# Kernel tuning notes

Measured on AMD Instinct MI355X. Metric: run time of the kernel, lower is better.

## Reference

```python
import jax, jax.numpy as jnp
import numpy as np
import math

MAX2D = 1001        # max_2d_position_embeddings
COORD = 128         # coordinate_size
SHAPE = 128         # shape_size
PE = 384            # pos_embed_size
HID = 768           # layout_hidden_size
PAD = 0             # pad_token_id
EPS = 1e-12
INIT = 1024         # sinusoidal init_size
BIG = 100000000


def sinusoidal_table(num_embeddings=INIT, dim=PE, padding_idx=PAD):
    half = dim // 2
    freq = np.exp(np.arange(half, dtype=np.float32) * (-math.log(10000.0) / (half - 1)))
    ang = np.arange(num_embeddings, dtype=np.float32)[:, None] * freq[None, :]
    tab = np.concatenate([np.sin(ang), np.cos(ang)], axis=1)
    if padding_idx is not None:
        tab[padding_idx, :] = 0.0
    return jnp.asarray(tab, dtype=jnp.float32)


def setup_inputs() -> dict:
    key = jax.random.key(0)
    ks = jax.random.split(key, 16)
    B, L = 2, 1024
    x1 = jax.random.randint(ks[0], (B, L), 0, 501, dtype=jnp.int32)
    y1 = jax.random.randint(ks[1], (B, L), 0, 501, dtype=jnp.int32)
    w = jax.random.randint(ks[2], (B, L), 0, 500, dtype=jnp.int32)
    h = jax.random.randint(ks[3], (B, L), 0, 500, dtype=jnp.int32)
    bbox = jnp.stack([x1, y1, x1 + w, y1 + h], axis=-1)  # [B,L,4], 0..1000
    attention_mask = jnp.ones((B, L), dtype=jnp.int32)
    s = 0.02
    inp = {
        'bbox': bbox,
        'attention_mask': attention_mask,
        'x_tab': jax.random.normal(ks[4], (MAX2D, COORD), jnp.float32) * s,
        'y_tab': jax.random.normal(ks[5], (MAX2D, COORD), jnp.float32) * s,
        'h_tab': jax.random.normal(ks[6], (MAX2D, SHAPE), jnp.float32) * s,
        'w_tab': jax.random.normal(ks[7], (MAX2D, SHAPE), jnp.float32) * s,
        'W_tl_w': jax.random.normal(ks[8], (HID, 2 * PE), jnp.float32) * s,
        'W_tl_b': jnp.zeros((HID,), jnp.float32),
        'W_tr_w': jax.random.normal(ks[9], (HID, 2 * PE), jnp.float32) * s,
        'W_tr_b': jnp.zeros((HID,), jnp.float32),
        'W_bl_w': jax.random.normal(ks[10], (HID, 2 * PE), jnp.float32) * s,
        'W_bl_b': jnp.zeros((HID,), jnp.float32),
        'W_br_w': jax.random.normal(ks[11], (HID, 2 * PE), jnp.float32) * s,
        'W_br_b': jnp.zeros((HID,), jnp.float32),
        'ln_g': jnp.ones((HID,), jnp.float32),
        'ln_b': jnp.zeros((HID,), jnp.float32),
        'params': 50,
    }
    return inp


def _knn_graph(bbox, mask, topk):
    # mask out padded boxes with a huge coordinate (matches masked_fill)
    bm = jnp.where((mask == 0)[..., None], BIG, bbox).astype(jnp.float32)
    xc = (bm[:, :, 0] + bm[:, :, 2]) / 2.0
    yc = (bm[:, :, 1] + bm[:, :, 3]) / 2.0
    dist = (xc[:, :, None] - xc[:, None, :]) ** 2 + (yc[:, :, None] - yc[:, None, :]) ** 2
    _, topk_index = jax.lax.top_k(-dist, topk)  # smallest distances
    topk_index = topk_index.astype(jnp.int32)
    B, L, _ = topk_index.shape
    lm = jnp.zeros((B, L, L), jnp.int32)
    b_ix = jnp.arange(B)[:, None, None]
    l_ix = jnp.arange(L)[None, :, None]
    lm = lm.at[b_ix, l_ix, topk_index].set(1)
    return topk_index, lm


def _rel_pos_emb(bbox, topk_index, sin_tab):
    # diff[b,i,k] = coord[b,i] - coord[b,topk_index[b,i,k]]
    gather = jax.vmap(lambda v, idx: v[idx])  # per-batch gather

    def diffs(c):
        d = c[:, :, None] - gather(c, topk_index)
        d = jnp.clip(d, 1 - MAX2D, MAX2D - 1)
        # torch negative indexing into the table wraps: idx % INIT
        return sin_tab[jnp.mod(d, INIT)]  # [B,L,K,PE]

    ex1 = diffs(bbox[:, :, 0])
    ey1 = diffs(bbox[:, :, 1])
    ex2 = diffs(bbox[:, :, 2])
    ey2 = diffs(bbox[:, :, 3])
    return ex1, ey1, ex2, ey2


def _linear(x, w, b):
    return jnp.einsum('blki,oi->blko', x, w) + b


def reference(bbox, attention_mask, x_tab, y_tab, h_tab, w_tab,
              W_tl_w, W_tl_b, W_tr_w, W_tr_b, W_bl_w, W_bl_b, W_br_w, W_br_b,
              ln_g, ln_b, params):
    sin_tab = sinusoidal_table()
    # spatial position embeddings
    layout_emb = jnp.concatenate([
        x_tab[bbox[:, :, 0]], y_tab[bbox[:, :, 1]],
        x_tab[bbox[:, :, 2]], y_tab[bbox[:, :, 3]],
        h_tab[bbox[:, :, 3] - bbox[:, :, 1]],
        w_tab[bbox[:, :, 2] - bbox[:, :, 0]],
    ], axis=-1)  # [B,L,HID]

    topk = min(bbox.shape[1], int(params))
    topk_index, local_mask = _knn_graph(bbox, attention_mask, topk)

    ex1, ey1, ex2, ey2 = _rel_pos_emb(bbox, topk_index, sin_tab)
    p = (_linear(jnp.concatenate([ex1, ey1], -1), W_tl_w, W_tl_b)
         + _linear(jnp.concatenate([ex2, ey1], -1), W_tr_w, W_tr_b)
         + _linear(jnp.concatenate([ex1, ey2], -1), W_bl_w, W_bl_b)
         + _linear(jnp.concatenate([ex2, ey2], -1), W_br_w, W_br_b))

    mu = jnp.mean(layout_emb, axis=-1, keepdims=True)
    var = jnp.mean((layout_emb - mu) ** 2, axis=-1, keepdims=True)
    layout_emb = (layout_emb - mu) / jnp.sqrt(var + EPS) * ln_g + ln_b
    # dropout is identity in eval mode
    return layout_emb, p, topk_index, local_mask
```

## Files before the change

kernel.cpp:

```cpp
#include <hip/hip_runtime.h>
#include <math.h>

namespace {
constexpr int B_ = 2;
constexpr int L_ = 1024;
constexpr int K_ = 50;
constexpr int HID_ = 768;
constexpr int PE_ = 384;
constexpr int HALF_ = 192;
constexpr int TROWS_ = 1024;

typedef float f32x4 __attribute__((ext_vector_type(4)));

constexpr long long OUT0 = 0;
constexpr long long OUT1 = OUT0 + (long long)B_ * L_ * HID_;
constexpr long long OUT2 = OUT1 + (long long)B_ * L_ * K_ * HID_;
constexpr long long OUT3 = OUT2 + (long long)B_ * L_ * K_;

constexpr long long WS_SIN = 0;
constexpr long long WS_T   = WS_SIN + (long long)TROWS_ * PE_;
constexpr long long WS_TI  = WS_T + 4LL * TROWS_ * HID_;

constexpr int GEMM_BLOCKS = 16 * 12 * 4;
constexpr int TOPK_BLOCKS = B_ * L_;
constexpr int LN_BLOCKS   = B_ * L_;
}

__global__ __launch_bounds__(192) void k_sin_tab(float* __restrict__ tab) {
    const int r = blockIdx.x;
    const int j = threadIdx.x;
    const float c = -0.04822168780092243f;
    float fr = expf((float)j * c);
    float ang = (float)r * fr;
    float s, co;
    if (r == 0) { s = 0.f; co = 0.f; } else { s = sinf(ang); co = cosf(ang); }
    tab[r * PE_ + j] = s;
    tab[r * PE_ + HALF_ + j] = co;
}

union SMem {
    struct { float As[32][68]; float Bs[32][68]; } g;
    struct { float xs[L_]; float ys[L_]; float mrow[L_];
             unsigned long long wmin[4]; } t;
    struct { float red[4]; } l;
};

__device__ __forceinline__ float block_sum_256(float x, float* red) {
    #pragma unroll
    for (int off = 32; off > 0; off >>= 1) x += __shfl_xor(x, off, 64);
    const int wave = threadIdx.x >> 6;
    if ((threadIdx.x & 63) == 0) red[wave] = x;
    __syncthreads();
    float t = red[0] + red[1] + red[2] + red[3];
    __syncthreads();
    return t;
}

__global__ __launch_bounds__(256) void k_mega(
    const float* __restrict__ sinT,
    const float* __restrict__ Wtl, const float* __restrict__ Wtr,
    const float* __restrict__ Wbl, const float* __restrict__ Wbr,
    const float* __restrict__ btl, const float* __restrict__ btr,
    const float* __restrict__ bbl, const float* __restrict__ bbr,
    float* __restrict__ Tout,
    const int4* __restrict__ bbox, const int* __restrict__ am,
    float* __restrict__ topk_f, int* __restrict__ topk_i, float* __restrict__ mask,
    const float* __restrict__ xt, const float* __restrict__ yt,
    const float* __restrict__ ht, const float* __restrict__ wt,
    const float* __restrict__ lng, const float* __restrict__ lnb,
    float* __restrict__ lout)
{
    __shared__ SMem sm;
    const int bid = blockIdx.x;
    const int tid = threadIdx.x;

    if (bid < GEMM_BLOCKS) {
        const int t   = bid / 192;
        const int rem = bid - t * 192;
        const int rx  = rem & 15;
        const int oy  = rem >> 4;
        const float* Wa; const float* Wb; int coff;
        if (t == 0)      { Wa = Wtl; Wb = Wbl; coff = 0; }
        else if (t == 1) { Wa = Wtr; Wb = Wbr; coff = 0; }
        else if (t == 2) { Wa = Wtl; Wb = Wtr; coff = PE_; }
        else             { Wa = Wbl; Wb = Wbr; coff = PE_; }

        const int r0 = rx * 64;
        const int o0 = oy * 64;
        const int ty = tid >> 4, tx = tid & 15;
        float acc[4][4] = {{0.f,0.f,0.f,0.f},{0.f,0.f,0.f,0.f},
                           {0.f,0.f,0.f,0.f},{0.f,0.f,0.f,0.f}};

        for (int k0 = 0; k0 < PE_; k0 += 32) {
            #pragma unroll
            for (int s = 0; s < 2; ++s) {
                int idx = s * 256 + tid;
                int rr = idx >> 3, q = idx & 7;
                f32x4 av = *(const f32x4*)&sinT[(r0 + rr) * PE_ + k0 + q * 4];
                f32x4 w1 = *(const f32x4*)&Wa[(o0 + rr) * (2 * PE_) + coff + k0 + q * 4];
                f32x4 w2 = *(const f32x4*)&Wb[(o0 + rr) * (2 * PE_) + coff + k0 + q * 4];
                f32x4 bv = w1 + w2;
                #pragma unroll
                for (int c = 0; c < 4; ++c) {
                    sm.g.As[q * 4 + c][rr] = av[c];
                    sm.g.Bs[q * 4 + c][rr] = bv[c];
                }
            }
            __syncthreads();
            #pragma unroll
            for (int kk = 0; kk < 32; ++kk) {
                f32x4 a = *(const f32x4*)&sm.g.As[kk][ty * 4];
                f32x4 b = *(const f32x4*)&sm.g.Bs[kk][tx * 4];
                #pragma unroll
                for (int m = 0; m < 4; ++m)
                    #pragma unroll
                    for (int n = 0; n < 4; ++n)
                        acc[m][n] = fmaf(a[m], b[n], acc[m][n]);
            }
            __syncthreads();
        }

        #pragma unroll
        for (int m = 0; m < 4; ++m) {
            int r = r0 + ty * 4 + m;
            f32x4 v;
            #pragma unroll
            for (int n = 0; n < 4; ++n) {
                int o = o0 + tx * 4 + n;
                float x = acc[m][n];
                if (t == 0) x += btl[o] + btr[o] + bbl[o] + bbr[o];
                v[n] = x;
            }
            *(f32x4*)&Tout[(long long)t * TROWS_ * HID_ + (long long)r * HID_ + o0 + tx * 4] = v;
        }
        return;
    }

    if (bid < GEMM_BLOCKS + TOPK_BLOCKS) {
        const int bi = bid - GEMM_BLOCKS;
        const int b = bi >> 10;
        const int i = bi & 1023;
        for (int j = tid; j < L_; j += 256) {
            int4 q = bbox[b * L_ + j];
            float x1, y1, x2, y2;
            if (am[b * L_ + j] == 0) { x1 = y1 = x2 = y2 = 1e8f; }
            else { x1 = (float)q.x; y1 = (float)q.y; x2 = (float)q.z; y2 = (float)q.w; }
            sm.t.xs[j] = (x1 + x2) * 0.5f;
            sm.t.ys[j] = (y1 + y2) * 0.5f;
            sm.t.mrow[j] = 0.f;
        }
        __syncthreads();
        const float xq = sm.t.xs[i], yq = sm.t.ys[i];
        unsigned long long key[4];
        #pragma unroll
        for (int s = 0; s < 4; ++s) {
            int j = tid + s * 256;
            float dx = xq - sm.t.xs[j], dy = yq - sm.t.ys[j];
            float d = dx * dx + dy * dy;
            key[s] = ((unsigned long long)__float_as_uint(d) << 32) | (unsigned int)j;
        }
        const int lane = tid & 63, wave = tid >> 6;
        const long long obase = (long long)(b * L_ + i) * K_;
        for (int r = 0; r < K_; ++r) {
            unsigned long long m = key[0] < key[1] ? key[0] : key[1];
            unsigned long long m2 = key[2] < key[3] ? key[2] : key[3];
            if (m2 < m) m = m2;
            #pragma unroll
            for (int off = 1; off < 64; off <<= 1) {
                unsigned long long o = __shfl_xor(m, off, 64);
                if (o < m) m = o;
            }
            if (lane == 0) sm.t.wmin[wave] = m;
            __syncthreads();
            unsigned long long mm = sm.t.wmin[0] < sm.t.wmin[1] ? sm.t.wmin[0] : sm.t.wmin[1];
            unsigned long long mb = sm.t.wmin[2] < sm.t.wmin[3] ? sm.t.wmin[2] : sm.t.wmin[3];
            if (mb < mm) mm = mb;
            if (tid == 0) {
                int w = (int)(mm & 0xffffffffu);
                topk_f[obase + r] = (float)w;
                topk_i[obase + r] = w;
                sm.t.mrow[w] = 1.0f;
            }
            #pragma unroll
            for (int s = 0; s < 4; ++s) if (key[s] == mm) key[s] = ~0ULL;
            __syncthreads();
        }
        f32x4* mrow = (f32x4*)(mask + (long long)(b * L_ + i) * L_);
        const f32x4* src = (const f32x4*)sm.t.mrow;
        __builtin_nontemporal_store(src[tid], mrow + tid);
        return;
    }

    {
        const int tok = bid - (GEMM_BLOCKS + TOPK_BLOCKS);
        const int4 q = bbox[tok];
        float v[3];
        #pragma unroll
        for (int s = 0; s < 3; ++s) {
            int e = tid + s * 256;
            int off = e & 127;
            int seg = e >> 7;
            float val;
            if (seg == 0)      val = xt[q.x * 128 + off];
            else if (seg == 1) val = yt[q.y * 128 + off];
            else if (seg == 2) val = xt[q.z * 128 + off];
            else if (seg == 3) val = yt[q.w * 128 + off];
            else if (seg == 4) val = ht[(q.w - q.y) * 128 + off];
            else               val = wt[(q.z - q.x) * 128 + off];
            v[s] = val;
        }
        float mu = block_sum_256(v[0] + v[1] + v[2], sm.l.red) * (1.0f / 768.0f);
        float sq = 0.f;
        #pragma unroll
        for (int s = 0; s < 3; ++s) { float d = v[s] - mu; sq = fmaf(d, d, sq); }
        float var = block_sum_256(sq, sm.l.red) * (1.0f / 768.0f);
        float inv = 1.0f / sqrtf(var + 1e-12f);
        float* orow = lout + (long long)tok * HID_;
        #pragma unroll
        for (int s = 0; s < 3; ++s) {
            int e = tid + s * 256;
            __builtin_nontemporal_store((v[s] - mu) * inv * lng[e] + lnb[e], orow + e);
        }
    }
}

__device__ __forceinline__ int wrapc(int d) {
    d = d < -1000 ? -1000 : (d > 1000 ? 1000 : d);
    return (d + 1024) & 1023;
}

__global__ __launch_bounds__(256) void k_passemble(
    const int4* __restrict__ bbox, const int* __restrict__ topk_i,
    const f32x4* __restrict__ T, float* __restrict__ p)
{
    const int row = blockIdx.x * 4 + (threadIdx.x >> 6);
    const int lane = threadIdx.x & 63;
    const int b = row / (L_ * K_);
    const int rem = row - b * (L_ * K_);
    const int i = rem / K_;
    const int j = topk_i[row];
    const int4 bi = bbox[b * L_ + i];
    const int4 bj = bbox[b * L_ + j];
    const f32x4* T1 = T + (long long)wrapc(bi.x - bj.x) * 192;
    const f32x4* T2 = T + 196608 + (long long)wrapc(bi.z - bj.z) * 192;
    const f32x4* T3 = T + 2 * 196608 + (long long)wrapc(bi.y - bj.y) * 192;
    const f32x4* T4 = T + 3 * 196608 + (long long)wrapc(bi.w - bj.w) * 192;
    f32x4* prow = (f32x4*)p + (long long)row * 192;
    #pragma unroll
    for (int u = 0; u < 3; ++u) {
        int f = lane + u * 64;
        f32x4 o = T1[f] + T2[f] + T3[f] + T4[f];
        __builtin_nontemporal_store(o, prow + f);
    }
}

extern "C" void kernel_launch(void* const* d_in, const int* in_sizes, int n_in,
                              void* d_out, int out_size, void* d_ws, size_t ws_size,
                              hipStream_t stream)
{
    const int4* bbox = (const int4*)d_in[0];
    const int* am    = (const int*)d_in[1];
    const float* xt  = (const float*)d_in[2];
    const float* yt  = (const float*)d_in[3];
    const float* ht  = (const float*)d_in[4];
    const float* wt  = (const float*)d_in[5];
    const float* Wtl = (const float*)d_in[6];
    const float* btl = (const float*)d_in[7];
    const float* Wtr = (const float*)d_in[8];
    const float* btr = (const float*)d_in[9];
    const float* Wbl = (const float*)d_in[10];
    const float* bbl = (const float*)d_in[11];
    const float* Wbr = (const float*)d_in[12];
    const float* bbr = (const float*)d_in[13];
    const float* lng = (const float*)d_in[14];
    const float* lnb = (const float*)d_in[15];

    float* out = (float*)d_out;
    float* ws = (float*)d_ws;
    float* sinT = ws + WS_SIN;
    float* T = ws + WS_T;
    int* topk_i = (int*)(ws + WS_TI);

    k_sin_tab<<<dim3(TROWS_), dim3(HALF_), 0, stream>>>(sinT);
    k_mega<<<dim3(GEMM_BLOCKS + TOPK_BLOCKS + LN_BLOCKS), dim3(256), 0, stream>>>(
        sinT, Wtl, Wtr, Wbl, Wbr, btl, btr, bbl, bbr, T,
        bbox, am, out + OUT2, topk_i, out + OUT3,
        xt, yt, ht, wt, lng, lnb, out + OUT0);
    k_passemble<<<dim3(B_ * L_ * K_ / 4), dim3(256), 0, stream>>>(
        bbox, topk_i, (const f32x4*)T, out + OUT1);
}
```

Before: 528.4 us.

## Store relative-position tables in fp16 and restructure GEMM with pre-transposed operands

```diff
diff --git a/kernel.cpp b/kernel.cpp
--- a/kernel.cpp
+++ b/kernel.cpp
@@ -11,35 +11,80 @@
 constexpr int TROWS_ = 1024;
 
 typedef float f32x4 __attribute__((ext_vector_type(4)));
+typedef _Float16 f16x4 __attribute__((ext_vector_type(4)));
+typedef _Float16 f16x8 __attribute__((ext_vector_type(8)));
 
 constexpr long long OUT0 = 0;
 constexpr long long OUT1 = OUT0 + (long long)B_ * L_ * HID_;
 constexpr long long OUT2 = OUT1 + (long long)B_ * L_ * K_ * HID_;
 constexpr long long OUT3 = OUT2 + (long long)B_ * L_ * K_;
 
-constexpr long long WS_SIN = 0;
-constexpr long long WS_T   = WS_SIN + (long long)TROWS_ * PE_;
-constexpr long long WS_TI  = WS_T + 4LL * TROWS_ * HID_;
-
-constexpr int GEMM_BLOCKS = 16 * 12 * 4;
+constexpr long long WS_ST = 0;
+constexpr long long WS_UT = WS_ST + (long long)PE_ * TROWS_;
+constexpr long long WS_T  = WS_UT + 4LL * PE_ * HID_;
+constexpr long long WS_TI = WS_T + 2LL * TROWS_ * HID_;
+
+constexpr int GEMM_BLOCKS = 8 * 6 * 4;
 constexpr int TOPK_BLOCKS = B_ * L_;
 constexpr int LN_BLOCKS   = B_ * L_;
 }
 
-__global__ __launch_bounds__(192) void k_sin_tab(float* __restrict__ tab) {
-    const int r = blockIdx.x;
-    const int j = threadIdx.x;
-    const float c = -0.04822168780092243f;
-    float fr = expf((float)j * c);
-    float ang = (float)r * fr;
-    float s, co;
-    if (r == 0) { s = 0.f; co = 0.f; } else { s = sinf(ang); co = cosf(ang); }
-    tab[r * PE_ + j] = s;
-    tab[r * PE_ + HALF_ + j] = co;
-}
-
-union SMem {
-    struct { float As[32][68]; float Bs[32][68]; } g;
+__global__ __launch_bounds__(256) void k_pre(
+    const float* __restrict__ Wtl, const float* __restrict__ Wtr,
+    const float* __restrict__ Wbl, const float* __restrict__ Wbr,
+    float* __restrict__ ST, float* __restrict__ UT)
+{
+    __shared__ float tile[64][68];
+    const int bid = blockIdx.x;
+    const int tid = threadIdx.x;
+
+    if (bid < PE_) {
+        const int jj = bid < HALF_ ? bid : bid - HALF_;
+        const float c = -0.04822168780092243f;
+        float fr = expf((float)jj * c);
+        #pragma unroll
+        for (int s = 0; s < 4; ++s) {
+            int r = tid + s * 256;
+            float ang = (float)r * fr;
+            float v;
+            if (r == 0) v = 0.f;
+            else        v = (bid < HALF_) ? sinf(ang) : cosf(ang);
+            ST[bid * TROWS_ + r] = v;
+        }
+        return;
+    }
+
+    int rem = bid - PE_;
+    const int t = rem / 72; rem -= t * 72;
+    const int o0 = (rem % 12) * 64;
+    const int j0 = (rem / 12) * 64;
+    const float* Wa; const float* Wb; int coff;
+    if (t == 0)      { Wa = Wtl; Wb = Wbl; coff = 0; }
+    else if (t == 1) { Wa = Wtr; Wb = Wbr; coff = 0; }
+    else if (t == 2) { Wa = Wtl; Wb = Wtr; coff = PE_; }
+    else             { Wa = Wbl; Wb = Wbr; coff = PE_; }
+
+    #pragma unroll
+    for (int p = 0; p < 4; ++p) {
+        int oo = (tid >> 4) + p * 16;
+        int jq = tid & 15;
+        f32x4 w1 = *(const f32x4*)&Wa[(long long)(o0 + oo) * (2 * PE_) + coff + j0 + jq * 4];
+        f32x4 w2 = *(const f32x4*)&Wb[(long long)(o0 + oo) * (2 * PE_) + coff + j0 + jq * 4];
+        f32x4 s = w1 + w2;
+        #pragma unroll
+        for (int c = 0; c < 4; ++c) tile[jq * 4 + c][oo] = s[c];
+    }
+    __syncthreads();
+    #pragma unroll
+    for (int p = 0; p < 4; ++p) {
+        int jj = (tid >> 4) + p * 16;
+        int oq = tid & 15;
+        f32x4 v = *(const f32x4*)&tile[jj][oq * 4];
+        *(f32x4*)&UT[((long long)t * PE_ + j0 + jj) * HID_ + o0 + oq * 4] = v;
+    }
+}
+
+union SMemM {
     struct { float xs[L_]; float ys[L_]; float mrow[L_];
              unsigned long long wmin[4]; } t;
     struct { float red[4]; } l;
@@ -56,13 +101,11 @@
     return t;
 }
 
-__global__ __launch_bounds__(256) void k_mega(
-    const float* __restrict__ sinT,
-    const float* __restrict__ Wtl, const float* __restrict__ Wtr,
-    const float* __restrict__ Wbl, const float* __restrict__ Wbr,
+__global__ __launch_bounds__(256, 4) void k_mega(
+    const float* __restrict__ ST, const float* __restrict__ UT,
     const float* __restrict__ btl, const float* __restrict__ btr,
     const float* __restrict__ bbl, const float* __restrict__ bbr,
-    float* __restrict__ Tout,
+    _Float16* __restrict__ Th,
     const int4* __restrict__ bbox, const int* __restrict__ am,
     float* __restrict__ topk_f, int* __restrict__ topk_i, float* __restrict__ mask,
     const float* __restrict__ xt, const float* __restrict__ yt,
@@ -70,68 +113,55 @@
     const float* __restrict__ lng, const float* __restrict__ lnb,
     float* __restrict__ lout)
 {
-    __shared__ SMem sm;
+    __shared__ SMemM sm;
     const int bid = blockIdx.x;
     const int tid = threadIdx.x;
 
     if (bid < GEMM_BLOCKS) {
-        const int t   = bid / 192;
-        const int rem = bid - t * 192;
-        const int rx  = rem & 15;
-        const int oy  = rem >> 4;
-        const float* Wa; const float* Wb; int coff;
-        if (t == 0)      { Wa = Wtl; Wb = Wbl; coff = 0; }
-        else if (t == 1) { Wa = Wtr; Wb = Wbr; coff = 0; }
-        else if (t == 2) { Wa = Wtl; Wb = Wtr; coff = PE_; }
-        else             { Wa = Wbl; Wb = Wbr; coff = PE_; }
-
-        const int r0 = rx * 64;
-        const int o0 = oy * 64;
+        const int t   = bid / 48;
+        const int rem = bid - t * 48;
+        const int r0  = (rem & 7) * 128;
+        const int o0  = (rem >> 3) * 128;
         const int ty = tid >> 4, tx = tid & 15;
-        float acc[4][4] = {{0.f,0.f,0.f,0.f},{0.f,0.f,0.f,0.f},
-                           {0.f,0.f,0.f,0.f},{0.f,0.f,0.f,0.f}};
-
-        for (int k0 = 0; k0 < PE_; k0 += 32) {
-            #pragma unroll
-            for (int s = 0; s < 2; ++s) {
-                int idx = s * 256 + tid;
-                int rr = idx >> 3, q = idx & 7;
-                f32x4 av = *(const f32x4*)&sinT[(r0 + rr) * PE_ + k0 + q * 4];
-                f32x4 w1 = *(const f32x4*)&Wa[(o0 + rr) * (2 * PE_) + coff + k0 + q * 4];
-                f32x4 w2 = *(const f32x4*)&Wb[(o0 + rr) * (2 * PE_) + coff + k0 + q * 4];
-                f32x4 bv = w1 + w2;
+
+        const float* A  = ST + r0 + ty * 8;
+        const float* Bp = UT + (long long)t * PE_ * HID_ + o0 + tx * 8;
+
+        float acc[8][8];
+        #pragma unroll
+        for (int m = 0; m < 8; ++m)
+            #pragma unroll
+            for (int n = 0; n < 8; ++n) acc[m][n] = 0.f;
+
+        #pragma unroll 2
+        for (int kk = 0; kk < PE_; ++kk) {
+            f32x4 a0 = *(const f32x4*)&A[(long long)kk * TROWS_];
+            f32x4 a1 = *(const f32x4*)&A[(long long)kk * TROWS_ + 4];
+            f32x4 b0 = *(const f32x4*)&Bp[(long long)kk * HID_];
+            f32x4 b1 = *(const f32x4*)&Bp[(long long)kk * HID_ + 4];
+            #pragma unroll
+            for (int m = 0; m < 8; ++m) {
+                float av = (m < 4) ? a0[m] : a1[m - 4];
                 #pragma unroll
-                for (int c = 0; c < 4; ++c) {
-                    sm.g.As[q * 4 + c][rr] = av[c];
-                    sm.g.Bs[q * 4 + c][rr] = bv[c];
+                for (int n = 0; n < 4; ++n) {
+                    acc[m][n]     = fmaf(av, b0[n], acc[m][n]);
+                    acc[m][n + 4] = fmaf(av, b1[n], acc[m][n + 4]);
                 }
             }
-            __syncthreads();
-            #pragma unroll
-            for (int kk = 0; kk < 32; ++kk) {
-                f32x4 a = *(const f32x4*)&sm.g.As[kk][ty * 4];
-                f32x4 b = *(const f32x4*)&sm.g.Bs[kk][tx * 4];
-                #pragma unroll
-                for (int m = 0; m < 4; ++m)
-                    #pragma unroll
-                    for (int n = 0; n < 4; ++n)
-                        acc[m][n] = fmaf(a[m], b[n], acc[m][n]);
-            }
-            __syncthreads();
-        }
-
-        #pragma unroll
-        for (int m = 0; m < 4; ++m) {
-            int r = r0 + ty * 4 + m;
-            f32x4 v;
-            #pragma unroll
-            for (int n = 0; n < 4; ++n) {
-                int o = o0 + tx * 4 + n;
+        }
+
+        #pragma unroll
+        for (int m = 0; m < 8; ++m) {
+            int r = r0 + ty * 8 + m;
+            f16x8 h;
+            #pragma unroll
+            for (int n = 0; n < 8; ++n) {
+                int o = o0 + tx * 8 + n;
                 float x = acc[m][n];
                 if (t == 0) x += btl[o] + btr[o] + bbl[o] + bbr[o];
-                v[n] = x;
+                h[n] = (_Float16)x;
             }
-            *(f32x4*)&Tout[(long long)t * TROWS_ * HID_ + (long long)r * HID_ + o0 + tx * 4] = v;
+            *(f16x8*)&Th[((long long)t * TROWS_ + r) * HID_ + o0 + tx * 8] = h;
         }
         return;
     }
@@ -231,7 +261,7 @@
 
 __global__ __launch_bounds__(256) void k_passemble(
     const int4* __restrict__ bbox, const int* __restrict__ topk_i,
-    const f32x4* __restrict__ T, float* __restrict__ p)
+    const _Float16* __restrict__ Th, float* __restrict__ p)
 {
     const int row = blockIdx.x * 4 + (threadIdx.x >> 6);
     const int lane = threadIdx.x & 63;
@@ -241,16 +271,24 @@
     const int j = topk_i[row];
     const int4 bi = bbox[b * L_ + i];
     const int4 bj = bbox[b * L_ + j];
-    const f32x4* T1 = T + (long long)wrapc(bi.x - bj.x) * 192;
-    const f32x4* T2 = T + 196608 + (long long)wrapc(bi.z - bj.z) * 192;
-    const f32x4* T3 = T + 2 * 196608 + (long long)wrapc(bi.y - bj.y) * 192;
-    const f32x4* T4 = T + 3 * 196608 + (long long)wrapc(bi.w - bj.w) * 192;
+    const _Float16* T1 = Th + (long long)wrapc(bi.x - bj.x) * HID_;
+    const _Float16* T2 = Th + 1LL * TROWS_ * HID_ + (long long)wrapc(bi.z - bj.z) * HID_;
+    const _Float16* T3 = Th + 2LL * TROWS_ * HID_ + (long long)wrapc(bi.y - bj.y) * HID_;
+    const _Float16* T4 = Th + 3LL * TROWS_ * HID_ + (long long)wrapc(bi.w - bj.w) * HID_;
     f32x4* prow = (f32x4*)p + (long long)row * 192;
     #pragma unroll
     for (int u = 0; u < 3; ++u) {
-        int f = lane + u * 64;
-        f32x4 o = T1[f] + T2[f] + T3[f] + T4[f];
-        __builtin_nontemporal_store(o, prow + f);
+        int fv = lane + u * 64;
+        int f = fv * 4;
+        f16x4 h1 = *(const f16x4*)&T1[f];
+        f16x4 h2 = *(const f16x4*)&T2[f];
+        f16x4 h3 = *(const f16x4*)&T3[f];
+        f16x4 h4 = *(const f16x4*)&T4[f];
+        f32x4 o;
+        #pragma unroll
+        for (int c = 0; c < 4; ++c)
+            o[c] = (float)h1[c] + (float)h2[c] + (float)h3[c] + (float)h4[c];
+        __builtin_nontemporal_store(o, prow + fv);
     }
 }
 
@@ -277,15 +315,16 @@
 
     float* out = (float*)d_out;
     float* ws = (float*)d_ws;
-    float* sinT = ws + WS_SIN;
-    float* T = ws + WS_T;
+    float* ST = ws + WS_ST;
+    float* UT = ws + WS_UT;
+    _Float16* Th = (_Float16*)(ws + WS_T);
     int* topk_i = (int*)(ws + WS_TI);
 
-    k_sin_tab<<<dim3(TROWS_), dim3(HALF_), 0, stream>>>(sinT);
+    k_pre<<<dim3(PE_ + 288), dim3(256), 0, stream>>>(Wtl, Wtr, Wbl, Wbr, ST, UT);
     k_mega<<<dim3(GEMM_BLOCKS + TOPK_BLOCKS + LN_BLOCKS), dim3(256), 0, stream>>>(
-        sinT, Wtl, Wtr, Wbl, Wbr, btl, btr, bbl, bbr, T,
+        ST, UT, btl, btr, bbl, bbr, Th,
         bbox, am, out + OUT2, topk_i, out + OUT3,
         xt, yt, ht, wt, lng, lnb, out + OUT0);
     k_passemble<<<dim3(B_ * L_ * K_ / 4), dim3(256), 0, stream>>>(
-        bbox, topk_i, (const f32x4*)T, out + OUT1);
-}
+        bbox, topk_i, Th, out + OUT1);
+}
```

After: 525.5 us. No clear change (-0.6%).
